# Kernel optimization log

Hardware: AMD Instinct MI355X
Metric: run time of the kernel (lower is better)

## Reference

```python
import jax, jax.numpy as jnp
import numpy as np

NUM_HEADS = 8
KERNEL_SEARCH = 5  # local attention window
EPS = 1e-5


def _layernorm(x, g, b):
    m = jnp.mean(x, axis=-1, keepdims=True)
    v = jnp.var(x, axis=-1, keepdims=True)
    return (x - m) / jnp.sqrt(v + EPS) * g + b


def _unfold3(x):
    # x: [N, C, H, W] -> [N, C*9, H*W]; matches torch F.unfold(kernel=3, pad=1)
    # ordering: channel-major, kernel position (row-major) minor.
    N, C, H, W = x.shape
    xp = jnp.pad(x, ((0, 0), (0, 0), (1, 1), (1, 1)))
    pats = jnp.stack([xp[:, :, i:i + H, j:j + W] for i in range(3) for j in range(3)], axis=2)
    return pats.reshape(N, C * 9, H * W)


def _sai2token(x, w_mlp):
    # x: [b, c, a, h, w] -> tokens [h*w, b*a, spa_dim]
    b, c, a, h, w = x.shape
    x = x.transpose(0, 2, 1, 3, 4).reshape(b * a, c, h, w)
    tok = _unfold3(x).transpose(2, 0, 1)  # [hw, b*a, c*9]
    return jnp.einsum('lnk,ek->lne', tok, w_mlp)


def _local_mask(h, w, k):
    # additive mask [h*w, h*w]: 0 inside local kxk window, -inf outside
    kl, kr = k // 2, k - k // 2
    ii = jnp.arange(h)
    jj = jnp.arange(w)
    okh = (ii[None, :] >= ii[:, None] - kl) & (ii[None, :] < ii[:, None] + kr)  # [h,h]
    okw = (jj[None, :] >= jj[:, None] - kl) & (jj[None, :] < jj[:, None] + kr)  # [w,w]
    ok = okh[:, None, :, None] & okw[None, :, None, :]  # [h,w,h,w]
    ok = ok.reshape(h * w, h * w)
    return jnp.where(ok, 0.0, -jnp.inf).astype(jnp.float32)


def _attention(qk_in, v_in, in_proj_w, out_proj_w, bias):
    # qk_in/v_in: [L, B, E]; torch nn.MultiheadAttention, no biases, eval mode
    L, B, E = qk_in.shape
    Dh = E // NUM_HEADS
    Wq, Wk, Wv = in_proj_w[:E], in_proj_w[E:2 * E], in_proj_w[2 * E:]
    q = jnp.einsum('lbe,fe->lbf', qk_in, Wq).reshape(L, B, NUM_HEADS, Dh)
    k = jnp.einsum('lbe,fe->lbf', qk_in, Wk).reshape(L, B, NUM_HEADS, Dh)
    v = jnp.einsum('lbe,fe->lbf', v_in, Wv).reshape(L, B, NUM_HEADS, Dh)
    scale = 1.0 / np.sqrt(Dh).astype(np.float32)
    scores = jnp.einsum('lbhd,mbhd->bhlm', q, k) * scale + bias[None, None]
    attn = jax.nn.softmax(scores, axis=-1)
    out = jnp.einsum('bhlm,mbhd->lbhd', attn, v).reshape(L, B, E)
    return jnp.einsum('lbe,fe->lbf', out, out_proj_w)


def reference(buffer, spa_position, w_mlp, ln1_g, ln1_b, in_proj_w, out_proj_w,
              ln2_g, ln2_b, ff_w1, ff_w2, conv_w):
    b, c, a, h, w = buffer.shape
    bias = _local_mask(h, w, KERNEL_SEARCH)
    tok = _sai2token(buffer, w_mlp)          # [hw, b*a, E]
    pe = _sai2token(spa_position, w_mlp)
    x = _layernorm(tok + pe, ln1_g, ln1_b)
    tok = _attention(x, tok, in_proj_w, out_proj_w, bias) + tok
    # feed-forward (dropout is identity in eval)
    ff = _layernorm(tok, ln2_g, ln2_b)
    ff = jax.nn.relu(jnp.einsum('lbe,fe->lbf', ff, ff_w1))
    tok = jnp.einsum('lbf,ef->lbe', ff, ff_w2) + tok
    # Token2SAI: '(h w) (b a) e -> b e a h w' then 1x1x1 conv3d
    buf = tok.reshape(h, w, b, a, -1).transpose(2, 4, 3, 0, 1)  # [b, E, a, h, w]
    return jnp.einsum('oe,beahw->boahw', conv_w, buf)


def setup_inputs() -> dict:
    key = jax.random.key(0)
    ks = jax.random.split(key, 8)
    b, c, a, h, w = 1, 64, 25, 32, 32
    E = 2 * c
    s = 0.02
    return {
        'buffer': jax.random.normal(ks[0], (b, c, a, h, w), jnp.float32),
        'spa_position': jax.random.normal(ks[1], (b, c, a, h, w), jnp.float32),
        'w_mlp': jax.random.normal(ks[2], (E, c * 9), jnp.float32) * s,
        'ln1_g': jnp.ones((E,), jnp.float32),
        'ln1_b': jnp.zeros((E,), jnp.float32),
        'in_proj_w': jax.random.normal(ks[3], (3 * E, E), jnp.float32) * s,
        'out_proj_w': jax.random.normal(ks[4], (E, E), jnp.float32) * s,
        'ln2_g': jnp.ones((E,), jnp.float32),
        'ln2_b': jnp.zeros((E,), jnp.float32),
        'ff_w1': jax.random.normal(ks[5], (2 * E, E), jnp.float32) * s,
        'ff_w2': jax.random.normal(ks[6], (E, 2 * E), jnp.float32) * s,
        'conv_w': jax.random.normal(ks[7], (c, E), jnp.float32) * s,
    }
```

## Files before the change

### kernel.cpp

```cpp
#include <hip/hip_runtime.h>
#include <math.h>

#define Lh 32
#define Lw 32
#define LL 1024
#define BN 25
#define EE 128
#define CC 64
#define NHD 8
#define DH 16
#define FFD 256
#define MROWS 25600

typedef __attribute__((ext_vector_type(8))) short short8;
typedef __attribute__((ext_vector_type(4))) float f32x4;

__device__ inline ushort f2b(float x) {
    union { float f; unsigned u; } v; v.f = x;
    unsigned r = (v.u + 0x7fffu + ((v.u >> 16) & 1u)) >> 16;
    return (ushort)r;
}
__device__ inline float b2f(ushort u) {
    union { unsigned u; float f; } v; v.u = ((unsigned)u) << 16;
    return v.f;
}

#define OFF_W2  0
#define OFF_WQK 73728
#define OFF_WV  106496
#define OFF_WO  122880
#define OFF_W1  139264
#define OFF_W2F 172032
#define OFF_WC  204800
#define W_TOTAL 212992

__global__ __launch_bounds__(256) void k_prep(
    const float* __restrict__ w_mlp, const float* __restrict__ in_proj,
    const float* __restrict__ out_proj, const float* __restrict__ ff_w1,
    const float* __restrict__ ff_w2, const float* __restrict__ conv_w,
    ushort* __restrict__ Wb)
{
    int i = blockIdx.x * 256 + threadIdx.x;
    if (i >= W_TOTAL) return;
    if (i < 73728) {
        int e = i / 576, k = i - e * 576;
        int tap = k >> 6, ch = k & 63;
        Wb[OFF_W2 + i] = f2b(w_mlp[e * 576 + ch * 9 + tap]);
        return;
    }
    i -= 73728;
    if (i < 32768) {
        float v = in_proj[i];
        Wb[OFF_WQK + i] = f2b(i < 16384 ? v * 0.25f : v);
        return;
    }
    i -= 32768;
    if (i < 16384) { Wb[OFF_WV + i] = f2b(in_proj[32768 + i]); return; }
    i -= 16384;
    if (i < 16384) {
        int e = i >> 7, kpos = i & 127;
        int c = kpos >> 5, q = (kpos >> 3) & 3, ii = kpos & 7;
        int orig = (2 * c + (ii >> 2)) * 16 + q * 4 + (ii & 3);
        Wb[OFF_WO + i] = f2b(out_proj[e * 128 + orig]);
        return;
    }
    i -= 16384;
    if (i < 32768) { Wb[OFF_W1 + i] = f2b(ff_w1[i]); return; }
    i -= 32768;
    if (i < 32768) {
        int e = i >> 8, kpos = i & 255;
        int c = kpos >> 5, q = (kpos >> 3) & 3, ii = kpos & 7;
        int orig = (2 * c + (ii >> 2)) * 16 + q * 4 + (ii & 3);
        Wb[OFF_W2F + i] = f2b(ff_w2[e * 256 + orig]);
        return;
    }
    i -= 32768;
    {
        int o = i >> 7, kpos = i & 127;
        int c = kpos >> 5, q = (kpos >> 3) & 3, ii = kpos & 7;
        int orig = (2 * c + (ii >> 2)) * 16 + q * 4 + (ii & 3);
        Wb[OFF_WC + i] = f2b(conv_w[o * 128 + orig]);
    }
}

__global__ __launch_bounds__(256, 3) void k_tok_qkv(
    const float* __restrict__ buf, const float* __restrict__ spa,
    const ushort* __restrict__ W2, const ushort* __restrict__ WQK,
    const ushort* __restrict__ WV, const float* __restrict__ g1,
    const float* __restrict__ b1, ushort* __restrict__ TOKb,
    ushort* __restrict__ Qh, ushort* __restrict__ Kh, ushort* __restrict__ VTg)
{
    const int bid = blockIdx.x;
    const int idx = (bid & 7) * 100 + (bid >> 3);
    const int n = idx / 32, y = idx & 31;
    __shared__ ushort At[3 * 34 * 72];
    __shared__ ushort As_[3 * 34 * 72];
    __shared__ ushort Xs[32 * 136];
    __shared__ ushort Vs[32 * 136];
    __shared__ float2 red[32][4];
    float* t0 = (float*)Xs;
    float* t1 = (float*)Vs;
    const int t = threadIdx.x;
    const uint4 z = make_uint4(0, 0, 0, 0);

    for (int dy = 0; dy < 3; dy++) {
        int yy = y + dy - 1;
        if (yy >= 0 && yy < Lh) {
            {
                int ch = t >> 2, x8 = (t & 3) * 8;
                const float* p = buf + ((size_t)(ch * BN + n) * LL + yy * Lw + x8);
                const float* q = spa + ((size_t)(ch * BN + n) * LL + yy * Lw + x8);
                float4 a0 = ((const float4*)p)[0], a1 = ((const float4*)p)[1];
                float4 b0 = ((const float4*)q)[0], b1 = ((const float4*)q)[1];
                float* d0 = t0 + ch * 33 + x8;
                float* d1 = t1 + ch * 33 + x8;
                d0[0] = a0.x; d0[1] = a0.y; d0[2] = a0.z; d0[3] = a0.w;
                d0[4] = a1.x; d0[5] = a1.y; d0[6] = a1.z; d0[7] = a1.w;
                d1[0] = a0.x + b0.x; d1[1] = a0.y + b0.y; d1[2] = a0.z + b0.z; d1[3] = a0.w + b0.w;
                d1[4] = a1.x + b1.x; d1[5] = a1.y + b1.y; d1[6] = a1.z + b1.z; d1[7] = a1.w + b1.w;
            }
            __syncthreads();
            {
                int x = t >> 3, c8 = (t & 7) * 8;
                union { ushort u[8]; uint4 v; } o0, o1;
#pragma unroll
                for (int j = 0; j < 8; j++) {
                    o0.u[j] = f2b(t0[(c8 + j) * 33 + x]);
                    o1.u[j] = f2b(t1[(c8 + j) * 33 + x]);
                }
                *(uint4*)(At + (dy * 34 + x + 1) * 72 + c8) = o0.v;
                *(uint4*)(As_ + (dy * 34 + x + 1) * 72 + c8) = o1.v;
            }
            __syncthreads();
        } else {
            int x = t >> 3, c8 = (t & 7) * 8;
            *(uint4*)(At + (dy * 34 + x + 1) * 72 + c8) = z;
            *(uint4*)(As_ + (dy * 34 + x + 1) * 72 + c8) = z;
        }
    }
    if (t < 48) {
        int dy = t / 16, rem = t % 16;
        int colp = (rem >> 3) * 33, c8p = (rem & 7) * 8;
        *(uint4*)(At + (dy * 34 + colp) * 72 + c8p) = z;
        *(uint4*)(As_ + (dy * 34 + colp) * 72 + c8p) = z;
    }
    __syncthreads();

    const int w = t >> 6, lane = t & 63;
    const int col = lane & 15, quad = lane >> 4;
    f32x4 accT[2][2] = {}, accS[2][2] = {};

    for (int tap = 0; tap < 9; tap++) {
        int dy = tap / 3, dx = tap % 3;
#pragma unroll
        for (int cc = 0; cc < 2; cc++) {
            int kg = tap * 64 + cc * 32 + quad * 8;
            short8 b0 = *(const short8*)(W2 + (size_t)(w * 32 + col) * 576 + kg);
            short8 bq = *(const short8*)(W2 + (size_t)(w * 32 + 16 + col) * 576 + kg);
            int abase = (dy * 34 + col + dx) * 72 + cc * 32 + quad * 8;
            short8 aT0 = *(const short8*)(At + abase);
            short8 aT1 = *(const short8*)(At + abase + 16 * 72);
            short8 aS0 = *(const short8*)(As_ + abase);
            short8 aS1 = *(const short8*)(As_ + abase + 16 * 72);
            accT[0][0] = __builtin_amdgcn_mfma_f32_16x16x32_bf16(aT0, b0, accT[0][0], 0, 0, 0);
            accT[0][1] = __builtin_amdgcn_mfma_f32_16x16x32_bf16(aT0, bq, accT[0][1], 0, 0, 0);
            accT[1][0] = __builtin_amdgcn_mfma_f32_16x16x32_bf16(aT1, b0, accT[1][0], 0, 0, 0);
            accT[1][1] = __builtin_amdgcn_mfma_f32_16x16x32_bf16(aT1, bq, accT[1][1], 0, 0, 0);
            accS[0][0] = __builtin_amdgcn_mfma_f32_16x16x32_bf16(aS0, b0, accS[0][0], 0, 0, 0);
            accS[0][1] = __builtin_amdgcn_mfma_f32_16x16x32_bf16(aS0, bq, accS[0][1], 0, 0, 0);
            accS[1][0] = __builtin_amdgcn_mfma_f32_16x16x32_bf16(aS1, b0, accS[1][0], 0, 0, 0);
            accS[1][1] = __builtin_amdgcn_mfma_f32_16x16x32_bf16(aS1, bq, accS[1][1], 0, 0, 0);
        }
    }

#pragma unroll
    for (int mi = 0; mi < 2; mi++)
#pragma unroll
        for (int r = 0; r < 4; r++) {
            float a0 = accS[mi][0][r], a1 = accS[mi][1][r];
            float ss = a0 + a1, qq = a0 * a0 + a1 * a1;
#pragma unroll
            for (int m = 1; m < 16; m <<= 1) {
                ss += __shfl_xor(ss, m, 64);
                qq += __shfl_xor(qq, m, 64);
            }
            if (col == 0) red[mi * 16 + quad * 4 + r][w] = make_float2(ss, qq);
        }
    __syncthreads();

    const float ga = g1[w * 32 + col],      ba = b1[w * 32 + col];
    const float gb = g1[w * 32 + 16 + col], bb = b1[w * 32 + 16 + col];
#pragma unroll
    for (int mi = 0; mi < 2; mi++)
#pragma unroll
        for (int r = 0; r < 4; r++) {
            int x = mi * 16 + quad * 4 + r;
            float2 p0 = red[x][0], p1 = red[x][1], p2 = red[x][2], p3 = red[x][3];
            float mean = (p0.x + p1.x + p2.x + p3.x) * (1.f / 128.f);
            float var  = (p0.y + p1.y + p2.y + p3.y) * (1.f / 128.f) - mean * mean;
            float rstd = rsqrtf(var + 1e-5f);
            int e0 = w * 32 + col, e1 = w * 32 + 16 + col;
            Xs[x * 136 + e0] = f2b((accS[mi][0][r] - mean) * rstd * ga + ba);
            Xs[x * 136 + e1] = f2b((accS[mi][1][r] - mean) * rstd * gb + bb);
            Vs[x * 136 + e0] = f2b(accT[mi][0][r]);
            Vs[x * 136 + e1] = f2b(accT[mi][1][r]);
        }
    __syncthreads();

    short8 xb[2][4], xv[2][4];
#pragma unroll
    for (int j = 0; j < 2; j++)
#pragma unroll
        for (int kc = 0; kc < 4; kc++) {
            xb[j][kc] = *(const short8*)(Xs + (j * 16 + col) * 136 + kc * 32 + quad * 8);
            xv[j][kc] = *(const short8*)(Vs + (j * 16 + col) * 136 + kc * 32 + quad * 8);
        }
    f32x4 Q[2][2] = {}, K[2][2] = {}, V[2][2] = {};
#pragma unroll
    for (int hj = 0; hj < 2; hj++) {
        int h = 2 * w + hj;
#pragma unroll
        for (int kc = 0; kc < 4; kc++) {
            short8 aq = *(const short8*)(WQK + (size_t)(h * 16 + col) * 128 + kc * 32 + quad * 8);
            short8 ak = *(const short8*)(WQK + (size_t)(128 + h * 16 + col) * 128 + kc * 32 + quad * 8);
            short8 av = *(const short8*)(WV + (size_t)(h * 16 + col) * 128 + kc * 32 + quad * 8);
#pragma unroll
            for (int j = 0; j < 2; j++) {
                Q[hj][j] = __builtin_amdgcn_mfma_f32_16x16x32_bf16(aq, xb[j][kc], Q[hj][j], 0, 0, 0);
                K[hj][j] = __builtin_amdgcn_mfma_f32_16x16x32_bf16(ak, xb[j][kc], K[hj][j], 0, 0, 0);
                V[hj][j] = __builtin_amdgcn_mfma_f32_16x16x32_bf16(av, xv[j][kc], V[hj][j], 0, 0, 0);
            }
        }
    }
    ushort* VTs = At;
#pragma unroll
    for (int hj = 0; hj < 2; hj++) {
        int h = 2 * w + hj;
#pragma unroll
        for (int j = 0; j < 2; j++) {
            int l = y * 32 + j * 16 + col;
            size_t base = ((size_t)(n * 8 + h) * 1024 + l) * 16 + quad * 4;
            ushort4 oq, ok;
            oq.x = f2b(Q[hj][j][0]); oq.y = f2b(Q[hj][j][1]); oq.z = f2b(Q[hj][j][2]); oq.w = f2b(Q[hj][j][3]);
            ok.x = f2b(K[hj][j][0]); ok.y = f2b(K[hj][j][1]); ok.z = f2b(K[hj][j][2]); ok.w = f2b(K[hj][j][3]);
            *(ushort4*)(Qh + base) = oq;
            *(ushort4*)(Kh + base) = ok;
            int xp = ((col >> 2) << 3) + (j << 2) + (col & 3);
#pragma unroll
            for (int r = 0; r < 4; r++)
                VTs[(h * 16 + quad * 4 + r) * 34 + xp] = f2b(V[hj][j][r]);
        }
    }
#pragma unroll
    for (int k = 0; k < 2; k++) {
        int idx2 = t + k * 256;
        int r = idx2 >> 4, seg = idx2 & 15;
        *(uint4*)(TOKb + ((size_t)((y * 32 + r) * 25 + n)) * 128 + seg * 8) =
            *(const uint4*)(Vs + r * 136 + seg * 8);
    }
    __syncthreads();
    {
        int h = t >> 5, rem = t & 31, d = rem >> 1, xh = (rem & 1) * 16;
        size_t vrow = ((size_t)(n * 8 + h) * 32 + y) * 512;
        union { ushort u[8]; uint4 v; } o0, o1;
#pragma unroll
        for (int j = 0; j < 8; j++) {
            o0.u[j] = VTs[(h * 16 + d) * 34 + xh + j];
            o1.u[j] = VTs[(h * 16 + d) * 34 + xh + 8 + j];
        }
        *(uint4*)(VTg + vrow + d * 32 + xh)     = o0.v;
        *(uint4*)(VTg + vrow + d * 32 + xh + 8) = o1.v;
    }
}

__global__ __launch_bounds__(256, 4) void k_attn_ffn(
    const ushort* __restrict__ Qh, const ushort* __restrict__ Kh,
    const ushort* __restrict__ VTg, const ushort* __restrict__ WOP,
    const float* __restrict__ g2, const float* __restrict__ b2,
    const ushort* __restrict__ W1, const ushort* __restrict__ W2P,
    const ushort* __restrict__ WCP, const ushort* __restrict__ TOKb,
    float* __restrict__ out)
{
    __shared__ ushort OX[32 * 136];
    __shared__ ushort Rs[32 * 136];
    __shared__ ushort Hs[32 * 264];
    __shared__ float2 red[32][4];
    ushort* Ys = Rs;
    const int bid = blockIdx.x;
    const int idx = (bid & 7) * 100 + (bid >> 3);
    const int n = idx / 32, y = idx & 31;
    const int t = threadIdx.x, w = t >> 6, lane = t & 63;
    const int col = lane & 15, quad = lane >> 4;

    {
#pragma unroll
        for (int k = 0; k < 2; k++) {
            int idx2 = t + k * 256;
            int r = idx2 >> 4, seg = idx2 & 15;
            *(uint4*)(Rs + r * 136 + seg * 8) =
                *(const uint4*)(TOKb + ((size_t)((y * 32 + r) * 25 + n)) * 128 + seg * 8);
        }
    }

    short8 z8 = {0, 0, 0, 0, 0, 0, 0, 0};
    const size_t base0 = (size_t)(n * 8 + 2 * w) * 1024;
    const size_t base1 = base0 + 1024;
    const size_t vbase0 = (size_t)(n * 8 + 2 * w) * 32 * 512;
    const size_t vbase1 = vbase0 + 32 * 512;

    short8 wop[2][4];

#pragma unroll
    for (int half = 0; half < 2; half++) {
        const int qx = half * 16 + col;
        unsigned long long mbits = 0;
#pragma unroll
        for (int tt = 0; tt < 10; tt++) {
            int yy = y - 2 + (tt >> 1);
            bool rok = (yy >= 0) && (yy < 32);
            int kxb = ((tt & 1) << 4) + quad * 4;
#pragma unroll
            for (int r = 0; r < 4; r++) {
                int dd = kxb + r - qx;
                if (rok && ((unsigned)(dd + 2) <= 4u))
                    mbits |= 1ull << (tt * 4 + r);
            }
        }

        short8 qf0 = z8, qf1 = z8;
        if (quad < 2) {
            qf0 = *(const short8*)(Qh + (base0 + y * 32 + half * 16 + col) * 16 + quad * 8);
            qf1 = *(const short8*)(Qh + (base1 + y * 32 + half * 16 + col) * 16 + quad * 8);
        }

        union { ushort u[8]; short8 s; } pb0[5], pb1[5];
        float sum0 = 0.f, sum1 = 0.f;
#pragma unroll
        for (int kr = 0; kr < 5; kr++) {
            int yyc = min(max(y - 2 + kr, 0), 31);
            short8 kf0a = z8, kf0b = z8, kf1a = z8, kf1b = z8;
            if (quad < 2) {
                kf0a = *(const short8*)(Kh + (base0 + yyc * 32 + col) * 16 + quad * 8);
                kf0b = *(const short8*)(Kh + (base0 + yyc * 32 + 16 + col) * 16 + quad * 8);
                kf1a = *(const short8*)(Kh + (base1 + yyc * 32 + col) * 16 + quad * 8);
                kf1b = *(const short8*)(Kh + (base1 + yyc * 32 + 16 + col) * 16 + quad * 8);
            }
            f32x4 S00 = {}, S01 = {}, S10 = {}, S11 = {};
            S00 = __builtin_amdgcn_mfma_f32_16x16x32_bf16(kf0a, qf0, S00, 0, 0, 0);
            S01 = __builtin_amdgcn_mfma_f32_16x16x32_bf16(kf0b, qf0, S01, 0, 0, 0);
            S10 = __builtin_amdgcn_mfma_f32_16x16x32_bf16(kf1a, qf1, S10, 0, 0, 0);
            S11 = __builtin_amdgcn_mfma_f32_16x16x32_bf16(kf1b, qf1, S11, 0, 0, 0);
#pragma unroll
            for (int i = 0; i < 8; i++) {
                int tt = 2 * kr + (i >> 2), r = i & 3;
                bool ok = (mbits >> (tt * 4 + r)) & 1;
                float s0 = (i >= 4) ? S01[r] : S00[r];
                float s1 = (i >= 4) ? S11[r] : S10[r];
                float p0 = ok ? __expf(s0) : 0.f;
                float p1 = ok ? __expf(s1) : 0.f;
                pb0[kr].u[i] = f2b(p0);
                pb1[kr].u[i] = f2b(p1);
                sum0 += p0; sum1 += p1;
            }
        }
        sum0 += __shfl_xor(sum0, 16, 64); sum0 += __shfl_xor(sum0, 32, 64);
        sum1 += __shfl_xor(sum1, 16, 64); sum1 += __shfl_xor(sum1, 32, 64);
        const float inv0 = 1.f / sum0, inv1 = 1.f / sum1;

        if (half == 1) {
#pragma unroll
            for (int jj = 0; jj < 2; jj++)
#pragma unroll
                for (int kc = 0; kc < 4; kc++)
                    wop[jj][kc] = *(const short8*)(WOP + (size_t)((2 * w + jj) * 16 + col) * 128 + kc * 32 + quad * 8);
        }

        f32x4 O20 = {}, O21 = {};
#pragma unroll
        for (int c = 0; c < 5; c++) {
            int yyc = min(max(y - 2 + c, 0), 31);
            short8 vt0 = *(const short8*)(VTg + vbase0 + (size_t)yyc * 512 + col * 32 + quad * 8);
            short8 vt1 = *(const short8*)(VTg + vbase1 + (size_t)yyc * 512 + col * 32 + quad * 8);
            O20 = __builtin_amdgcn_mfma_f32_16x16x32_bf16(vt0, pb0[c].s, O20, 0, 0, 0);
            O21 = __builtin_amdgcn_mfma_f32_16x16x32_bf16(vt1, pb1[c].s, O21, 0, 0, 0);
        }
#pragma unroll
        for (int r = 0; r < 4; r++) { O20[r] *= inv0; O21[r] *= inv1; }

        union { ushort u[8]; uint4 v; } pk;
#pragma unroll
        for (int i = 0; i < 4; i++) { pk.u[i] = f2b(O20[i]); pk.u[4 + i] = f2b(O21[i]); }
        *(uint4*)(OX + (half * 16 + col) * 136 + w * 32 + quad * 8) = pk.v;
    }
    __syncthreads();

    f32x4 Y[2][2] = {};
#pragma unroll
    for (int kc = 0; kc < 4; kc++) {
        short8 hb0 = *(const short8*)(OX + col * 136 + kc * 32 + quad * 8);
        short8 hb1 = *(const short8*)(OX + (16 + col) * 136 + kc * 32 + quad * 8);
#pragma unroll
        for (int jj = 0; jj < 2; jj++) {
            Y[jj][0] = __builtin_amdgcn_mfma_f32_16x16x32_bf16(wop[jj][kc], hb0, Y[jj][0], 0, 0, 0);
            Y[jj][1] = __builtin_amdgcn_mfma_f32_16x16x32_bf16(wop[jj][kc], hb1, Y[jj][1], 0, 0, 0);
        }
    }

    short8 w1p[2][4];
#pragma unroll
    for (int j2 = 0; j2 < 2; j2++)
#pragma unroll
        for (int kc = 0; kc < 4; kc++)
            w1p[j2][kc] = *(const short8*)(W1 + (size_t)((4 * w + j2) * 16 + col) * 128 + kc * 32 + quad * 8);

#pragma unroll
    for (int tt = 0; tt < 2; tt++) {
        float sum = 0.f, sq = 0.f;
#pragma unroll
        for (int jj = 0; jj < 2; jj++)
#pragma unroll
            for (int r = 0; r < 4; r++) {
                int e = (2 * w + jj) * 16 + quad * 4 + r;
                float v = Y[jj][tt][r] + b2f(Rs[(tt * 16 + col) * 136 + e]);
                Y[jj][tt][r] = v;
                sum += v; sq += v * v;
            }
        sum += __shfl_xor(sum, 16, 64); sum += __shfl_xor(sum, 32, 64);
        sq  += __shfl_xor(sq, 16, 64);  sq  += __shfl_xor(sq, 32, 64);
        if (quad == 0) red[tt * 16 + col][w] = make_float2(sum, sq);
    }
    __syncthreads();

#pragma unroll
    for (int tt = 0; tt < 2; tt++) {
        int tok = tt * 16 + col;
        float2 p0 = red[tok][0], p1 = red[tok][1], p2 = red[tok][2], p3 = red[tok][3];
        float mean = (p0.x + p1.x + p2.x + p3.x) * (1.f / 128.f);
        float var  = (p0.y + p1.y + p2.y + p3.y) * (1.f / 128.f) - mean * mean;
        float rstd = rsqrtf(var + 1e-5f);
#pragma unroll
        for (int jj = 0; jj < 2; jj++)
#pragma unroll
            for (int r = 0; r < 4; r++) {
                int e = (2 * w + jj) * 16 + quad * 4 + r;
                OX[tok * 136 + e] = f2b((Y[jj][tt][r] - mean) * rstd * g2[e] + b2[e]);
            }
    }
    __syncthreads();

#pragma unroll
    for (int tt = 0; tt < 2; tt++) {
        short8 xb[4];
#pragma unroll
        for (int kc = 0; kc < 4; kc++)
            xb[kc] = *(const short8*)(OX + (tt * 16 + col) * 136 + kc * 32 + quad * 8);
        f32x4 H[4] = {};
#pragma unroll
        for (int j = 0; j < 4; j++) {
#pragma unroll
            for (int kc = 0; kc < 4; kc++) {
                short8 a = (j < 2) ? w1p[j][kc]
                         : *(const short8*)(W1 + (size_t)((4 * w + j) * 16 + col) * 128 + kc * 32 + quad * 8);
                H[j] = __builtin_amdgcn_mfma_f32_16x16x32_bf16(a, xb[kc], H[j], 0, 0, 0);
            }
        }
#pragma unroll
        for (int cc = 0; cc < 2; cc++) {
            union { ushort u[8]; uint4 v; } pk;
#pragma unroll
            for (int i = 0; i < 8; i++)
                pk.u[i] = f2b(fmaxf(H[2 * cc + (i >> 2)][i & 3], 0.f));
            *(uint4*)(Hs + (tt * 16 + col) * 264 + (2 * w + cc) * 32 + quad * 8) = pk.v;
        }
    }

    short8 w2pp[2][4];
#pragma unroll
    for (int j = 0; j < 2; j++)
#pragma unroll
        for (int kc = 0; kc < 4; kc++)
            w2pp[j][kc] = *(const short8*)(W2P + (size_t)((2 * w + j) * 16 + col) * 256 + kc * 32 + quad * 8);
    __syncthreads();

    f32x4 Y2[2][2] = {};
#pragma unroll
    for (int kc = 0; kc < 8; kc++) {
        short8 hb0 = *(const short8*)(Hs + col * 264 + kc * 32 + quad * 8);
        short8 hb1 = *(const short8*)(Hs + (16 + col) * 264 + kc * 32 + quad * 8);
#pragma unroll
        for (int j = 0; j < 2; j++) {
            short8 a = (kc < 4) ? w2pp[j][kc]
                     : *(const short8*)(W2P + (size_t)((2 * w + j) * 16 + col) * 256 + kc * 32 + quad * 8);
            Y2[j][0] = __builtin_amdgcn_mfma_f32_16x16x32_bf16(a, hb0, Y2[j][0], 0, 0, 0);
            Y2[j][1] = __builtin_amdgcn_mfma_f32_16x16x32_bf16(a, hb1, Y2[j][1], 0, 0, 0);
        }
    }

    short8 wcp[4];
#pragma unroll
    for (int c = 0; c < 4; c++)
        wcp[c] = *(const short8*)(WCP + (size_t)(w * 16 + col) * 128 + c * 32 + quad * 8);

#pragma unroll
    for (int tt = 0; tt < 2; tt++) {
        union { ushort u[8]; uint4 v; } pk;
#pragma unroll
        for (int i = 0; i < 8; i++)
            pk.u[i] = f2b(Y2[i >> 2][tt][i & 3] + Y[i >> 2][tt][i & 3]);
        *(uint4*)(Ys + (tt * 16 + col) * 136 + w * 32 + quad * 8) = pk.v;
    }
    __syncthreads();

    f32x4 O[2] = {};
#pragma unroll
    for (int c = 0; c < 4; c++) {
        short8 yb0 = *(const short8*)(Ys + col * 136 + c * 32 + quad * 8);
        short8 yb1 = *(const short8*)(Ys + (16 + col) * 136 + c * 32 + quad * 8);
        O[0] = __builtin_amdgcn_mfma_f32_16x16x32_bf16(wcp[c], yb0, O[0], 0, 0, 0);
        O[1] = __builtin_amdgcn_mfma_f32_16x16x32_bf16(wcp[c], yb1, O[1], 0, 0, 0);
    }
#pragma unroll
    for (int tt = 0; tt < 2; tt++) {
        int l = y * 32 + tt * 16 + col;
#pragma unroll
        for (int r2 = 0; r2 < 4; r2++) {
            int o = w * 16 + quad * 4 + r2;
            out[(size_t)(o * 25 + n) * 1024 + l] = O[tt][r2];
        }
    }
}

extern "C" void kernel_launch(void* const* d_in, const int* in_sizes, int n_in,
                              void* d_out, int out_size, void* d_ws, size_t ws_size,
                              hipStream_t stream)
{
    const float* buffer   = (const float*)d_in[0];
    const float* spa      = (const float*)d_in[1];
    const float* w_mlp    = (const float*)d_in[2];
    const float* ln1_g    = (const float*)d_in[3];
    const float* ln1_b    = (const float*)d_in[4];
    const float* in_proj  = (const float*)d_in[5];
    const float* out_proj = (const float*)d_in[6];
    const float* ln2_g    = (const float*)d_in[7];
    const float* ln2_b    = (const float*)d_in[8];
    const float* ff_w1    = (const float*)d_in[9];
    const float* ff_w2    = (const float*)d_in[10];
    const float* conv_w   = (const float*)d_in[11];
    float* out = (float*)d_out;

    char* ws = (char*)d_ws;
    ushort* TOKb = (ushort*)(ws);
    ushort* Qh   = (ushort*)(ws + 6553600);
    ushort* Kh   = (ushort*)(ws + 13107200);
    ushort* VTg  = (ushort*)(ws + 19660800);
    ushort* Wb   = (ushort*)(ws + 26214400);

    k_prep<<<dim3((W_TOTAL + 255) / 256), 256, 0, stream>>>(
        w_mlp, in_proj, out_proj, ff_w1, ff_w2, conv_w, Wb);
    k_tok_qkv<<<dim3(800), 256, 0, stream>>>(buffer, spa, Wb + OFF_W2,
                                             Wb + OFF_WQK, Wb + OFF_WV,
                                             ln1_g, ln1_b, TOKb, Qh, Kh, VTg);
    k_attn_ffn<<<dim3(800), 256, 0, stream>>>(Qh, Kh, VTg, Wb + OFF_WO,
                                              ln2_g, ln2_b, Wb + OFF_W1,
                                              Wb + OFF_W2F, Wb + OFF_WC,
                                              TOKb, out);
}
```

Baseline: 160.5 us.

## Raise k_tok_qkv occupancy by shrinking LDS and register footprint

Raises the launch-bounds occupancy hint for k_tok_qkv from 3 to 4 blocks per CU. To fit, the staging tiles now convert to bf16 before the LDS write and alias existing buffers: Xs reuses As_ and a single VsBuf holds both staging tiles. The QKV MFMA loop is restructured to handle one 16-row j-slice at a time, which cuts live accumulator and operand registers. The cost is reloading the weight fragments for each j, and more register or scratch pressure under the tighter bound. Aliasing Xs onto As_ is also only safe if As_ is dead by then.

```diff
diff --git a/kernel.cpp b/kernel.cpp
--- a/kernel.cpp
+++ b/kernel.cpp
@@ -83,7 +83,7 @@
     }
 }
 
-__global__ __launch_bounds__(256, 3) void k_tok_qkv(
+__global__ __launch_bounds__(256, 4) void k_tok_qkv(
     const float* __restrict__ buf, const float* __restrict__ spa,
     const ushort* __restrict__ W2, const ushort* __restrict__ WQK,
     const ushort* __restrict__ WV, const float* __restrict__ g1,
@@ -95,11 +95,12 @@
     const int n = idx / 32, y = idx & 31;
     __shared__ ushort At[3 * 34 * 72];
     __shared__ ushort As_[3 * 34 * 72];
-    __shared__ ushort Xs[32 * 136];
-    __shared__ ushort Vs[32 * 136];
+    __shared__ ushort VsBuf[32 * 136];
     __shared__ float2 red[32][4];
-    float* t0 = (float*)Xs;
-    float* t1 = (float*)Vs;
+    ushort* Xs  = As_;
+    ushort* Vs  = VsBuf;
+    ushort* t0b = VsBuf;
+    ushort* t1b = VsBuf + 64 * 34;
     const int t = threadIdx.x;
     const uint4 z = make_uint4(0, 0, 0, 0);
 
@@ -112,12 +113,17 @@
                 const float* q = spa + ((size_t)(ch * BN + n) * LL + yy * Lw + x8);
                 float4 a0 = ((const float4*)p)[0], a1 = ((const float4*)p)[1];
                 float4 b0 = ((const float4*)q)[0], b1 = ((const float4*)q)[1];
-                float* d0 = t0 + ch * 33 + x8;
-                float* d1 = t1 + ch * 33 + x8;
-                d0[0] = a0.x; d0[1] = a0.y; d0[2] = a0.z; d0[3] = a0.w;
-                d0[4] = a1.x; d0[5] = a1.y; d0[6] = a1.z; d0[7] = a1.w;
-                d1[0] = a0.x + b0.x; d1[1] = a0.y + b0.y; d1[2] = a0.z + b0.z; d1[3] = a0.w + b0.w;
-                d1[4] = a1.x + b1.x; d1[5] = a1.y + b1.y; d1[6] = a1.z + b1.z; d1[7] = a1.w + b1.w;
+                union { ushort u[8]; uint w[4]; } o0, o1;
+                o0.u[0] = f2b(a0.x); o0.u[1] = f2b(a0.y); o0.u[2] = f2b(a0.z); o0.u[3] = f2b(a0.w);
+                o0.u[4] = f2b(a1.x); o0.u[5] = f2b(a1.y); o0.u[6] = f2b(a1.z); o0.u[7] = f2b(a1.w);
+                o1.u[0] = f2b(a0.x + b0.x); o1.u[1] = f2b(a0.y + b0.y);
+                o1.u[2] = f2b(a0.z + b0.z); o1.u[3] = f2b(a0.w + b0.w);
+                o1.u[4] = f2b(a1.x + b1.x); o1.u[5] = f2b(a1.y + b1.y);
+                o1.u[6] = f2b(a1.z + b1.z); o1.u[7] = f2b(a1.w + b1.w);
+                uint* d0 = (uint*)(t0b + ch * 34 + x8);
+                uint* d1 = (uint*)(t1b + ch * 34 + x8);
+#pragma unroll
+                for (int k = 0; k < 4; k++) { d0[k] = o0.w[k]; d1[k] = o1.w[k]; }
             }
             __syncthreads();
             {
@@ -125,8 +131,8 @@
                 union { ushort u[8]; uint4 v; } o0, o1;
 #pragma unroll
                 for (int j = 0; j < 8; j++) {
-                    o0.u[j] = f2b(t0[(c8 + j) * 33 + x]);
-                    o1.u[j] = f2b(t1[(c8 + j) * 33 + x]);
+                    o0.u[j] = t0b[(c8 + j) * 34 + x];
+                    o1.u[j] = t1b[(c8 + j) * 34 + x];
                 }
                 *(uint4*)(At + (dy * 34 + x + 1) * 72 + c8) = o0.v;
                 *(uint4*)(As_ + (dy * 34 + x + 1) * 72 + c8) = o1.v;
@@ -207,48 +213,43 @@
         }
     __syncthreads();
 
-    short8 xb[2][4], xv[2][4];
-#pragma unroll
-    for (int j = 0; j < 2; j++)
+    ushort* VTs = At;
+#pragma unroll
+    for (int j = 0; j < 2; j++) {
+        short8 xb[4], xv[4];
 #pragma unroll
         for (int kc = 0; kc < 4; kc++) {
-            xb[j][kc] = *(const short8*)(Xs + (j * 16 + col) * 136 + kc * 32 + quad * 8);
-            xv[j][kc] = *(const short8*)(Vs + (j * 16 + col) * 136 + kc * 32 + quad * 8);
-        }
-    f32x4 Q[2][2] = {}, K[2][2] = {}, V[2][2] = {};
-#pragma unroll
-    for (int hj = 0; hj < 2; hj++) {
-        int h = 2 * w + hj;
-#pragma unroll
-        for (int kc = 0; kc < 4; kc++) {
-            short8 aq = *(const short8*)(WQK + (size_t)(h * 16 + col) * 128 + kc * 32 + quad * 8);
-            short8 ak = *(const short8*)(WQK + (size_t)(128 + h * 16 + col) * 128 + kc * 32 + quad * 8);
-            short8 av = *(const short8*)(WV + (size_t)(h * 16 + col) * 128 + kc * 32 + quad * 8);
-#pragma unroll
-            for (int j = 0; j < 2; j++) {
-                Q[hj][j] = __builtin_amdgcn_mfma_f32_16x16x32_bf16(aq, xb[j][kc], Q[hj][j], 0, 0, 0);
-                K[hj][j] = __builtin_amdgcn_mfma_f32_16x16x32_bf16(ak, xb[j][kc], K[hj][j], 0, 0, 0);
-                V[hj][j] = __builtin_amdgcn_mfma_f32_16x16x32_bf16(av, xv[j][kc], V[hj][j], 0, 0, 0);
-            }
-        }
-    }
-    ushort* VTs = At;
-#pragma unroll
-    for (int hj = 0; hj < 2; hj++) {
-        int h = 2 * w + hj;
-#pragma unroll
-        for (int j = 0; j < 2; j++) {
+            xb[kc] = *(const short8*)(Xs + (j * 16 + col) * 136 + kc * 32 + quad * 8);
+            xv[kc] = *(const short8*)(Vs + (j * 16 + col) * 136 + kc * 32 + quad * 8);
+        }
+        f32x4 Qr[2] = {}, Kr[2] = {}, Vr[2] = {};
+#pragma unroll
+        for (int hj = 0; hj < 2; hj++) {
+            int h = 2 * w + hj;
+#pragma unroll
+            for (int kc = 0; kc < 4; kc++) {
+                short8 aq = *(const short8*)(WQK + (size_t)(h * 16 + col) * 128 + kc * 32 + quad * 8);
+                short8 ak = *(const short8*)(WQK + (size_t)(128 + h * 16 + col) * 128 + kc * 32 + quad * 8);
+                short8 av = *(const short8*)(WV + (size_t)(h * 16 + col) * 128 + kc * 32 + quad * 8);
+                Qr[hj] = __builtin_amdgcn_mfma_f32_16x16x32_bf16(aq, xb[kc], Qr[hj], 0, 0, 0);
+                Kr[hj] = __builtin_amdgcn_mfma_f32_16x16x32_bf16(ak, xb[kc], Kr[hj], 0, 0, 0);
+                Vr[hj] = __builtin_amdgcn_mfma_f32_16x16x32_bf16(av, xv[kc], Vr[hj], 0, 0, 0);
+            }
+        }
+#pragma unroll
+        for (int hj = 0; hj < 2; hj++) {
+            int h = 2 * w + hj;
             int l = y * 32 + j * 16 + col;
             size_t base = ((size_t)(n * 8 + h) * 1024 + l) * 16 + quad * 4;
             ushort4 oq, ok;
-            oq.x = f2b(Q[hj][j][0]); oq.y = f2b(Q[hj][j][1]); oq.z = f2b(Q[hj][j][2]); oq.w = f2b(Q[hj][j][3]);
-            ok.x = f2b(K[hj][j][0]); ok.y = f2b(K[hj][j][1]); ok.z = f2b(K[hj][j][2]); ok.w = f2b(K[hj][j][3]);
+            oq.x = f2b(Qr[hj][0]); oq.y = f2b(Qr[hj][1]); oq.z = f2b(Qr[hj][2]); oq.w = f2b(Qr[hj][3]);
+            ok.x = f2b(Kr[hj][0]); ok.y = f2b(Kr[hj][1]); ok.z = f2b(Kr[hj][2]); ok.w = f2b(Kr[hj][3]);
             *(ushort4*)(Qh + base) = oq;
             *(ushort4*)(Kh + base) = ok;
             int xp = ((col >> 2) << 3) + (j << 2) + (col & 3);
 #pragma unroll
             for (int r = 0; r < 4; r++)
-                VTs[(h * 16 + quad * 4 + r) * 34 + xp] = f2b(V[hj][j][r]);
+                VTs[(h * 16 + quad * 4 + r) * 34 + xp] = f2b(Vr[hj][r]);
         }
     }
 #pragma unroll
```

New measurement: 165.4 us. 3.0% more time.
